# Optimization experiments

Measured on AMD Instinct MI355X. Metric: run time of the kernel, lower is better.

Reference implementation:

```python
import jax, jax.numpy as jnp
import numpy as np

B, N, F_IN, F_OUT = 8, 2048, 256, 64
ALPHA = 0.2          # LeakyReLU negative slope
NEG_INF = -9e15      # matches -9000000000000000.0 in the torch code


def setup_inputs() -> dict:
    key = jax.random.key(0)
    k = jax.random.split(key, 7)
    x = jax.random.normal(k[0], (B, N, F_IN), dtype=jnp.float32)
    adj = jax.random.randint(k[1], (B, N, N), 0, 2, dtype=jnp.int32)
    # W: nn.Linear(in_features, out_features)
    W = jax.random.normal(k[2], (F_IN, F_OUT), dtype=jnp.float32) / np.sqrt(F_IN)
    b_W = jax.random.normal(k[3], (F_OUT,), dtype=jnp.float32) * 0.01
    # a: nn.Linear(2*out_features, 1); decomposed as a_src (first F_OUT rows,
    # multiplies h_i) and a_dst (last F_OUT rows, multiplies h_j) + bias.
    a_src = jax.random.normal(k[4], (F_OUT,), dtype=jnp.float32) / np.sqrt(2 * F_OUT)
    a_dst = jax.random.normal(k[5], (F_OUT,), dtype=jnp.float32) / np.sqrt(2 * F_OUT)
    a_b = jax.random.normal(k[6], (), dtype=jnp.float32) * 0.01
    return {"x": x, "adj": adj, "W": W, "b_W": b_W,
            "a_src": a_src, "a_dst": a_dst, "a_b": a_b}


def reference(x, adj, W, b_W, a_src, a_dst, a_b):
    # h = W(input): [B, N, F_OUT]
    h = jnp.einsum('bnf,fo->bno', x, W) + b_W
    # Additive attention decomposition: a([h_i || h_j]) = a_src.h_i + a_dst.h_j + b
    # (avoids materializing the [B, N, N, 2F] concat tensor of the original)
    src = jnp.einsum('bno,o->bn', h, a_src)  # row term  (h_i)
    dst = jnp.einsum('bno,o->bn', h, a_dst)  # col term  (h_j)
    e = jax.nn.leaky_relu(src[:, :, None] + dst[:, None, :] + a_b, ALPHA)  # [B,N,N]
    e = jnp.where(adj > 0, e, NEG_INF)
    attention = jax.nn.softmax(e, axis=2)
    h_prime = jnp.einsum('bij,bjo->bio', attention, h)  # [B, N, F_OUT]
    return jax.nn.elu(h_prime)  # concat=True branch
```

## Files before the change

kernel.cpp:

```cpp
#include <hip/hip_runtime.h>

#define B_   8
#define N_   2048
#define FIN  256
#define FOUT 64
#define ALPHA 0.2f

typedef __attribute__((ext_vector_type(8))) short bf16x8;
typedef __attribute__((ext_vector_type(8))) unsigned short u16x8;
typedef __attribute__((ext_vector_type(4))) float f32x4;

__device__ __forceinline__ float b2f(unsigned short u) {
    union { unsigned int u; float f; } v; v.u = ((unsigned int)u) << 16; return v.f;
}
__device__ __forceinline__ unsigned short f2b(float f) {
    union { float f; unsigned int u; } v; v.f = f;
    unsigned int r = v.u + 0x7FFFu + ((v.u >> 16) & 1u);
    return (unsigned short)(r >> 16);
}

__global__ __launch_bounds__(256) void k_hgemm(
    const float* __restrict__ x, const float* __restrict__ W,
    const float* __restrict__ bW, unsigned short* __restrict__ h)
{
    const int tid = threadIdx.x;
    const int wv = tid >> 6, lane = tid & 63;
    const int quad = lane >> 4, col = lane & 15;
    const int f = wv * 16 + col;

    bf16x8 Bf[8];
    #pragma unroll
    for (int kk = 0; kk < 8; ++kk) {
        bf16x8 t;
        #pragma unroll
        for (int j = 0; j < 8; ++j)
            t[j] = (short)f2b(W[(kk * 32 + quad * 8 + j) * FOUT + f]);
        Bf[kk] = t;
    }
    const float bias = bW[f];
    const int rowbase = blockIdx.x * 64;
    #pragma unroll
    for (int rt = 0; rt < 4; ++rt) {
        const int r0 = rowbase + rt * 16;
        f32x4 acc = {0.f, 0.f, 0.f, 0.f};
        #pragma unroll
        for (int kk = 0; kk < 8; ++kk) {
            const float* xp = x + (size_t)(r0 + col) * FIN + kk * 32 + quad * 8;
            float4 x0 = *(const float4*)xp;
            float4 x1 = *(const float4*)(xp + 4);
            bf16x8 Af;
            Af[0] = (short)f2b(x0.x); Af[1] = (short)f2b(x0.y);
            Af[2] = (short)f2b(x0.z); Af[3] = (short)f2b(x0.w);
            Af[4] = (short)f2b(x1.x); Af[5] = (short)f2b(x1.y);
            Af[6] = (short)f2b(x1.z); Af[7] = (short)f2b(x1.w);
            acc = __builtin_amdgcn_mfma_f32_16x16x32_bf16(Af, Bf[kk], acc, 0, 0, 0);
        }
        #pragma unroll
        for (int reg = 0; reg < 4; ++reg) {
            int r = r0 + quad * 4 + reg;
            h[(size_t)r * FOUT + f] = f2b(acc[reg] + bias);
        }
    }
}

__global__ __launch_bounds__(256) void k_attn(
    const int* __restrict__ adj, const unsigned short* __restrict__ h,
    const float* __restrict__ asrc, const float* __restrict__ adst,
    const float* __restrict__ abp, float* __restrict__ out)
{
    __shared__ unsigned short h_s[128 * 72];
    __shared__ unsigned short w_s[32 * 136];
    __shared__ float dst_s[128];
    __shared__ float src_s[32];
    __shared__ float l_s[32];
    __shared__ float ad_s[FOUT];

    const int tid = threadIdx.x;
    const int wv = tid >> 6, lane = tid & 63;
    const int quad = lane >> 4, col = lane & 15;
    const int b = blockIdx.x >> 6;
    const int i0 = (blockIdx.x & 63) * 32;

    if (tid < FOUT) ad_s[tid] = adst[tid];
    {
        const int il = tid >> 3, fo = (tid & 7) * 8;
        u16x8 hv = *(const u16x8*)(h + (size_t)(b * N_ + i0 + il) * FOUT + fo);
        float s = 0.f;
        #pragma unroll
        for (int k = 0; k < 8; ++k) s += b2f(hv[k]) * asrc[fo + k];
        s += __shfl_xor(s, 1); s += __shfl_xor(s, 2); s += __shfl_xor(s, 4);
        if ((tid & 7) == 0) src_s[il] = s;
    }
    __syncthreads();

    const int il = tid >> 3, jg = tid & 7;
    const float srci = src_s[il] + abp[0];
    const int jl = tid >> 1, half = tid & 1;
    const int* adjbase = adj + (size_t)(b * N_ + i0 + il) * N_ + jg * 16;

    float lsum = 0.f;
    f32x4 acc0 = {0, 0, 0, 0}, acc1 = {0, 0, 0, 0};

    for (int jt = 0; jt < 16; ++jt) {
        const int j0 = jt * 128;
        {
            const unsigned short* hp = h + (size_t)(b * N_ + j0 + jl) * FOUT + half * 32;
            u16x8 va = *(const u16x8*)hp;
            u16x8 vb = *(const u16x8*)(hp + 8);
            u16x8 vc = *(const u16x8*)(hp + 16);
            u16x8 vd = *(const u16x8*)(hp + 24);
            unsigned short* q = &h_s[jl * 72 + half * 32];
            *(u16x8*)q = va; *(u16x8*)(q + 8) = vb;
            *(u16x8*)(q + 16) = vc; *(u16x8*)(q + 24) = vd;
        }
        __syncthreads();
        {
            float dsum = 0.f;
            #pragma unroll
            for (int k = 0; k < 32; ++k)
                dsum += b2f(h_s[jl * 72 + half * 32 + k]) * ad_s[half * 32 + k];
            dsum += __shfl_xor(dsum, 1);
            if (half == 0) dst_s[jl] = dsum;
        }
        __syncthreads();
        {
            const int* ap = adjbase + j0;
            int4 a0 = *(const int4*)ap;
            int4 a1 = *(const int4*)(ap + 4);
            int4 a2 = *(const int4*)(ap + 8);
            int4 a3 = *(const int4*)(ap + 12);
            int av[16] = {a0.x, a0.y, a0.z, a0.w, a1.x, a1.y, a1.z, a1.w,
                          a2.x, a2.y, a2.z, a2.w, a3.x, a3.y, a3.z, a3.w};
            u16x8 p0, p1;
            float ls = 0.f;
            #pragma unroll
            for (int k = 0; k < 16; ++k) {
                float e = srci + dst_s[jg * 16 + k];
                e = e > 0.f ? e : ALPHA * e;
                float wval = av[k] > 0 ? __expf(e) : 0.f;
                unsigned short wb = f2b(wval);
                ls += b2f(wb);
                if (k < 8) p0[k] = wb; else p1[k - 8] = wb;
            }
            lsum += ls;
            unsigned short* q = &w_s[il * 136 + jg * 16];
            *(u16x8*)q = p0; *(u16x8*)(q + 8) = p1;
        }
        __syncthreads();
        {
            #pragma unroll
            for (int kk = 0; kk < 4; ++kk) {
                bf16x8 Bf;
                #pragma unroll
                for (int jj = 0; jj < 8; ++jj)
                    Bf[jj] = (short)h_s[(kk * 32 + quad * 8 + jj) * 72 + wv * 16 + col];
                bf16x8 A0 = *(const bf16x8*)&w_s[col * 136 + kk * 32 + quad * 8];
                bf16x8 A1 = *(const bf16x8*)&w_s[(16 + col) * 136 + kk * 32 + quad * 8];
                acc0 = __builtin_amdgcn_mfma_f32_16x16x32_bf16(A0, Bf, acc0, 0, 0, 0);
                acc1 = __builtin_amdgcn_mfma_f32_16x16x32_bf16(A1, Bf, acc1, 0, 0, 0);
            }
        }
        __syncthreads();
    }

    lsum += __shfl_xor(lsum, 1);
    lsum += __shfl_xor(lsum, 2);
    lsum += __shfl_xor(lsum, 4);
    if (jg == 0) l_s[il] = lsum;
    __syncthreads();

    #pragma unroll
    for (int m = 0; m < 2; ++m) {
        f32x4 a = m ? acc1 : acc0;
        #pragma unroll
        for (int reg = 0; reg < 4; ++reg) {
            int row = m * 16 + quad * 4 + reg;
            float l = l_s[row];
            l = l > 0.f ? l : 1.f;
            float v = a[reg] / l;
            v = v > 0.f ? v : (__expf(v) - 1.f);
            out[(size_t)(b * N_ + i0 + row) * FOUT + wv * 16 + col] = v;
        }
    }
}

extern "C" void kernel_launch(void* const* d_in, const int* in_sizes, int n_in,
                              void* d_out, int out_size, void* d_ws, size_t ws_size,
                              hipStream_t stream)
{
    const float* x    = (const float*)d_in[0];
    const int*   adj  = (const int*)d_in[1];
    const float* W    = (const float*)d_in[2];
    const float* bW   = (const float*)d_in[3];
    const float* asrc = (const float*)d_in[4];
    const float* adst = (const float*)d_in[5];
    const float* abp  = (const float*)d_in[6];
    float* out = (float*)d_out;

    unsigned short* h = (unsigned short*)d_ws;

    k_hgemm<<<256, 256, 0, stream>>>(x, W, bW, h);
    k_attn<<<512, 256, 0, stream>>>(adj, h, asrc, adst, abp, out);
}
```

Measured before the change: 236.9 us.

## Precompute src/dst and transposed h, double-buffer attention tiles with register prefetch

Adds a kernel that computes the src and dst attention scores once per node and writes a feature-major transposed copy of h. The attention kernel then skips its per-tile recomputation of dst, reads the B operand with vector LDS loads instead of scalar gathers, and double-buffers the h and weight tiles in shared memory. Next-tile adj, h and dst values are prefetched into registers during the MFMA phase, and the iteration drops from four barriers to one. The cost is an extra launch, extra workspace traffic, and more registers and LDS per block.

```diff
diff --git a/kernel.cpp b/kernel.cpp
--- a/kernel.cpp
+++ b/kernel.cpp
@@ -63,17 +63,61 @@
     }
 }
 
+__global__ __launch_bounds__(256) void k_tr_srcdst(
+    const unsigned short* __restrict__ h,
+    const float* __restrict__ asrc, const float* __restrict__ adst,
+    unsigned short* __restrict__ hT, float* __restrict__ src, float* __restrict__ dst)
+{
+    __shared__ float as_s[FOUT], ad_s[FOUT];
+    __shared__ unsigned short tileT[FOUT * 72];
+    const int tid = threadIdx.x;
+    if (tid < FOUT) { as_s[tid] = asrc[tid]; ad_s[tid] = adst[tid]; }
+    __syncthreads();
+    const int r0 = blockIdx.x * 64;
+    const int b = r0 >> 11;
+    const int j0b = r0 & (N_ - 1);
+    {
+        const int i = tid >> 2, fb = (tid & 3) * 16;
+        const unsigned short* hp = h + (size_t)(r0 + i) * FOUT + fb;
+        u16x8 v0 = *(const u16x8*)hp;
+        u16x8 v1 = *(const u16x8*)(hp + 8);
+        float sp = 0.f, dp = 0.f;
+        #pragma unroll
+        for (int k = 0; k < 8; ++k) {
+            float hv = b2f(v0[k]);
+            sp += hv * as_s[fb + k]; dp += hv * ad_s[fb + k];
+            tileT[(fb + k) * 72 + i] = v0[k];
+        }
+        #pragma unroll
+        for (int k = 0; k < 8; ++k) {
+            float hv = b2f(v1[k]);
+            sp += hv * as_s[fb + 8 + k]; dp += hv * ad_s[fb + 8 + k];
+            tileT[(fb + 8 + k) * 72 + i] = v1[k];
+        }
+        sp += __shfl_xor(sp, 1); sp += __shfl_xor(sp, 2);
+        dp += __shfl_xor(dp, 1); dp += __shfl_xor(dp, 2);
+        if ((tid & 3) == 0) { src[r0 + i] = sp; dst[r0 + i] = dp; }
+    }
+    __syncthreads();
+    {
+        const int fq = tid >> 2, ic = (tid & 3) * 16;
+        u16x8 o0 = *(const u16x8*)&tileT[fq * 72 + ic];
+        u16x8 o1 = *(const u16x8*)&tileT[fq * 72 + ic + 8];
+        unsigned short* op = hT + (size_t)(b * FOUT + fq) * N_ + j0b + ic;
+        *(u16x8*)op = o0;
+        *(u16x8*)(op + 8) = o1;
+    }
+}
+
 __global__ __launch_bounds__(256) void k_attn(
-    const int* __restrict__ adj, const unsigned short* __restrict__ h,
-    const float* __restrict__ asrc, const float* __restrict__ adst,
-    const float* __restrict__ abp, float* __restrict__ out)
-{
-    __shared__ unsigned short h_s[128 * 72];
-    __shared__ unsigned short w_s[32 * 136];
-    __shared__ float dst_s[128];
+    const int* __restrict__ adj, const float* __restrict__ src, const float* __restrict__ dst,
+    const unsigned short* __restrict__ hT, const float* __restrict__ abp,
+    float* __restrict__ out)
+{
+    __shared__ unsigned short h_s[2][64 * 136];
+    __shared__ unsigned short w_s[2][32 * 136];
     __shared__ float src_s[32];
     __shared__ float l_s[32];
-    __shared__ float ad_s[FOUT];
 
     const int tid = threadIdx.x;
     const int wv = tid >> 6, lane = tid & 63;
@@ -81,61 +125,49 @@
     const int b = blockIdx.x >> 6;
     const int i0 = (blockIdx.x & 63) * 32;
 
-    if (tid < FOUT) ad_s[tid] = adst[tid];
-    {
-        const int il = tid >> 3, fo = (tid & 7) * 8;
-        u16x8 hv = *(const u16x8*)(h + (size_t)(b * N_ + i0 + il) * FOUT + fo);
-        float s = 0.f;
-        #pragma unroll
-        for (int k = 0; k < 8; ++k) s += b2f(hv[k]) * asrc[fo + k];
-        s += __shfl_xor(s, 1); s += __shfl_xor(s, 2); s += __shfl_xor(s, 4);
-        if ((tid & 7) == 0) src_s[il] = s;
-    }
+    if (tid < 32) src_s[tid] = src[b * N_ + i0 + tid];
     __syncthreads();
 
     const int il = tid >> 3, jg = tid & 7;
     const float srci = src_s[il] + abp[0];
-    const int jl = tid >> 1, half = tid & 1;
+    const int fq = tid >> 2, q4 = tid & 3;
+    const unsigned short* hTbase = hT + (size_t)(b * FOUT + fq) * N_ + q4 * 32;
     const int* adjbase = adj + (size_t)(b * N_ + i0 + il) * N_ + jg * 16;
+    const float* dstbase = dst + b * N_ + jg * 16;
+
+    u16x8 hv0 = *(const u16x8*)(hTbase);
+    u16x8 hv1 = *(const u16x8*)(hTbase + 8);
+    u16x8 hv2 = *(const u16x8*)(hTbase + 16);
+    u16x8 hv3 = *(const u16x8*)(hTbase + 24);
+    int4 a0 = *(const int4*)(adjbase);
+    int4 a1 = *(const int4*)(adjbase + 4);
+    int4 a2 = *(const int4*)(adjbase + 8);
+    int4 a3 = *(const int4*)(adjbase + 12);
+    float4 d0 = *(const float4*)(dstbase);
+    float4 d1 = *(const float4*)(dstbase + 4);
+    float4 d2 = *(const float4*)(dstbase + 8);
+    float4 d3 = *(const float4*)(dstbase + 12);
 
     float lsum = 0.f;
     f32x4 acc0 = {0, 0, 0, 0}, acc1 = {0, 0, 0, 0};
 
     for (int jt = 0; jt < 16; ++jt) {
-        const int j0 = jt * 128;
-        {
-            const unsigned short* hp = h + (size_t)(b * N_ + j0 + jl) * FOUT + half * 32;
-            u16x8 va = *(const u16x8*)hp;
-            u16x8 vb = *(const u16x8*)(hp + 8);
-            u16x8 vc = *(const u16x8*)(hp + 16);
-            u16x8 vd = *(const u16x8*)(hp + 24);
-            unsigned short* q = &h_s[jl * 72 + half * 32];
-            *(u16x8*)q = va; *(u16x8*)(q + 8) = vb;
-            *(u16x8*)(q + 16) = vc; *(u16x8*)(q + 24) = vd;
-        }
-        __syncthreads();
-        {
-            float dsum = 0.f;
-            #pragma unroll
-            for (int k = 0; k < 32; ++k)
-                dsum += b2f(h_s[jl * 72 + half * 32 + k]) * ad_s[half * 32 + k];
-            dsum += __shfl_xor(dsum, 1);
-            if (half == 0) dst_s[jl] = dsum;
-        }
-        __syncthreads();
-        {
-            const int* ap = adjbase + j0;
-            int4 a0 = *(const int4*)ap;
-            int4 a1 = *(const int4*)(ap + 4);
-            int4 a2 = *(const int4*)(ap + 8);
-            int4 a3 = *(const int4*)(ap + 12);
+        const int buf = jt & 1;
+        {
+            unsigned short* q = &h_s[buf][fq * 136 + q4 * 32];
+            *(u16x8*)q = hv0; *(u16x8*)(q + 8) = hv1;
+            *(u16x8*)(q + 16) = hv2; *(u16x8*)(q + 24) = hv3;
+        }
+        {
             int av[16] = {a0.x, a0.y, a0.z, a0.w, a1.x, a1.y, a1.z, a1.w,
                           a2.x, a2.y, a2.z, a2.w, a3.x, a3.y, a3.z, a3.w};
+            float dv[16] = {d0.x, d0.y, d0.z, d0.w, d1.x, d1.y, d1.z, d1.w,
+                            d2.x, d2.y, d2.z, d2.w, d3.x, d3.y, d3.z, d3.w};
             u16x8 p0, p1;
             float ls = 0.f;
             #pragma unroll
             for (int k = 0; k < 16; ++k) {
-                float e = srci + dst_s[jg * 16 + k];
+                float e = srci + dv[k];
                 e = e > 0.f ? e : ALPHA * e;
                 float wval = av[k] > 0 ? __expf(e) : 0.f;
                 unsigned short wb = f2b(wval);
@@ -143,24 +175,35 @@
                 if (k < 8) p0[k] = wb; else p1[k - 8] = wb;
             }
             lsum += ls;
-            unsigned short* q = &w_s[il * 136 + jg * 16];
+            unsigned short* q = &w_s[buf][il * 136 + jg * 16];
             *(u16x8*)q = p0; *(u16x8*)(q + 8) = p1;
         }
         __syncthreads();
+        {
+            const int jn = (jt < 15) ? (jt + 1) * 128 : 0;
+            hv0 = *(const u16x8*)(hTbase + jn);
+            hv1 = *(const u16x8*)(hTbase + jn + 8);
+            hv2 = *(const u16x8*)(hTbase + jn + 16);
+            hv3 = *(const u16x8*)(hTbase + jn + 24);
+            a0 = *(const int4*)(adjbase + jn);
+            a1 = *(const int4*)(adjbase + jn + 4);
+            a2 = *(const int4*)(adjbase + jn + 8);
+            a3 = *(const int4*)(adjbase + jn + 12);
+            d0 = *(const float4*)(dstbase + jn);
+            d1 = *(const float4*)(dstbase + jn + 4);
+            d2 = *(const float4*)(dstbase + jn + 8);
+            d3 = *(const float4*)(dstbase + jn + 12);
+        }
         {
             #pragma unroll
             for (int kk = 0; kk < 4; ++kk) {
-                bf16x8 Bf;
-                #pragma unroll
-                for (int jj = 0; jj < 8; ++jj)
-                    Bf[jj] = (short)h_s[(kk * 32 + quad * 8 + jj) * 72 + wv * 16 + col];
-                bf16x8 A0 = *(const bf16x8*)&w_s[col * 136 + kk * 32 + quad * 8];
-                bf16x8 A1 = *(const bf16x8*)&w_s[(16 + col) * 136 + kk * 32 + quad * 8];
+                bf16x8 A0 = *(const bf16x8*)&w_s[buf][col * 136 + kk * 32 + quad * 8];
+                bf16x8 A1 = *(const bf16x8*)&w_s[buf][(16 + col) * 136 + kk * 32 + quad * 8];
+                bf16x8 Bf = *(const bf16x8*)&h_s[buf][(wv * 16 + col) * 136 + kk * 32 + quad * 8];
                 acc0 = __builtin_amdgcn_mfma_f32_16x16x32_bf16(A0, Bf, acc0, 0, 0, 0);
                 acc1 = __builtin_amdgcn_mfma_f32_16x16x32_bf16(A1, Bf, acc1, 0, 0, 0);
             }
         }
-        __syncthreads();
     }
 
     lsum += __shfl_xor(lsum, 1);
@@ -197,8 +240,13 @@
     const float* abp  = (const float*)d_in[6];
     float* out = (float*)d_out;
 
-    unsigned short* h = (unsigned short*)d_ws;
+    char* ws = (char*)d_ws;
+    unsigned short* h  = (unsigned short*)ws;
+    unsigned short* hT = (unsigned short*)(ws + (size_t)2 * 1024 * 1024);
+    float* src = (float*)(ws + (size_t)4 * 1024 * 1024);
+    float* dst = (float*)(ws + (size_t)4 * 1024 * 1024 + 64 * 1024);
 
     k_hgemm<<<256, 256, 0, stream>>>(x, W, bW, h);
-    k_attn<<<512, 256, 0, stream>>>(adj, h, asrc, adst, abp, out);
-}
+    k_tr_srcdst<<<256, 256, 0, stream>>>(h, asrc, adst, hT, src, dst);
+    k_attn<<<512, 256, 0, stream>>>(adj, src, dst, hT, abp, out);
+}
```

After: 222.8 us. 1.06x faster.
